# Optimization experiments

Measured on AMD Instinct MI355X. Metric: run time of the kernel, lower is better.

## Reference

```python
import jax, jax.numpy as jnp
import numpy as np

C_FINE, C_MID, C_COARSE = 100, 20, 5
EPS = 1e-12


def setup_inputs() -> dict:
    key = jax.random.key(0)
    k1, k2 = jax.random.split(key)
    N, D = 262144, 128
    representations = jax.random.normal(k1, (N, D), dtype=jnp.float32)
    target_fine = jax.random.randint(k2, (N,), 0, C_FINE, dtype=jnp.int32)
    # nested hierarchy: fine -> mid (5 fines per mid), fine -> coarse (20 fines per coarse)
    fine2mid = (jnp.arange(C_FINE, dtype=jnp.int32) // (C_FINE // C_MID)).astype(jnp.int32)
    fine2coarse = (jnp.arange(C_FINE, dtype=jnp.int32) // (C_FINE // C_COARSE)).astype(jnp.int32)
    return {
        "representations": representations,
        "target_fine": target_fine,
        "fine2mid": fine2mid,
        "fine2coarse": fine2coarse,
    }


def _safe_norm(diff):
    # L2 norm along last axis; eps gives a 0 subgradient at diff==0
    return jnp.sqrt(jnp.sum(diff * diff, axis=-1) + EPS)


def _segment_mean(x, ids, num_segments):
    ones = jnp.ones(x.shape[:1], x.dtype)
    s = jax.ops.segment_sum(x, ids, num_segments=num_segments)
    c = jax.ops.segment_sum(ones, ids, num_segments=num_segments)
    return s / jnp.maximum(c, 1.0)[:, None]


def reference(representations, target_fine, fine2mid, fine2coarse):
    # ---- tree construction (vectorized version of the per-class Python loops) ----
    # fine prototypes: mean of representations per fine class  [C_FINE, D]
    fine_protos = _segment_mean(representations, target_fine, C_FINE)
    # mid prototypes: mean of child fine prototypes  [C_MID, D]
    mid_protos = _segment_mean(fine_protos, fine2mid, C_MID)
    # coarse prototypes: mean of child mid prototypes  [C_COARSE, D]
    mid2coarse = jax.ops.segment_max(fine2coarse, fine2mid, num_segments=C_MID)
    coarse_protos = _segment_mean(mid_protos, mid2coarse, C_COARSE)
    # (the root node contributes ||root - root|| = 0 to every pair, so it is omitted)

    # ---- pairwise tree-path distances over all fine-class pairs ----
    iu, ju = np.triu_indices(C_FINE, k=1)  # static C*(C-1)/2 = 4950 pairs
    ci, cj = fine2coarse[iu], fine2coarse[ju]
    mi, mj = fine2mid[iu], fine2mid[ju]
    tree_d = _safe_norm(coarse_protos[ci] - coarse_protos[cj]) \
           + _safe_norm(mid_protos[mi] - mid_protos[mj])
    # Euclidean distances between fine prototypes
    proto_d = _safe_norm(fine_protos[iu] - fine_protos[ju])

    # ---- CPCC: loss = 1 - Pearson correlation(tree_d, proto_d) ----
    tc = tree_d - jnp.mean(tree_d)
    pc = proto_d - jnp.mean(proto_d)
    corr = jnp.sum(tc * pc) / jnp.sqrt(jnp.sum(tc * tc) * jnp.sum(pc * pc) + EPS)
    return 1.0 - corr
```

## Files before the change

### kernel.cpp

```cpp
#include <hip/hip_runtime.h>
#include <math.h>

#define C_FINE   100
#define C_MID    20
#define C_COARSE 5
#define D        128
#define NROWS    262144
#define NPAIRS   4950
#define NBLK4    78

#define NBS      256
#define NBD      16
#define CAP      4096

#define FP_OFF    0
#define DM_OFF    12800
#define DC_OFF    13200
#define ACC_OFF   13232
#define DONE_OFF  13244
#define FSUM_OFF  13248
#define CUR_OFF   26048
#define RIDX_OFF  26176

__global__ __launch_bounds__(128) void kZ_zero(float* __restrict__ ws) {
    const int t = threadIdx.x;
    if (t < C_FINE) ((int*)ws + CUR_OFF)[t] = 0;
}

__global__ __launch_bounds__(256) void kS_scatter(const int* __restrict__ tgt,
                                                  float* __restrict__ ws) {
    __shared__ int hist[C_FINE];
    __shared__ int cnt[C_FINE];
    __shared__ int gb[C_FINE];
    const int t = threadIdx.x, b = blockIdx.x;
    if (t < C_FINE) { hist[t] = 0; cnt[t] = 0; }
    if (t < 50) ws[FSUM_OFF + b * 50 + t] = 0.f;
    __syncthreads();

    const int4 cs = ((const int4*)tgt)[b * 256 + t];
    atomicAdd(&hist[cs.x], 1); atomicAdd(&hist[cs.y], 1);
    atomicAdd(&hist[cs.z], 1); atomicAdd(&hist[cs.w], 1);
    __syncthreads();

    int* curs = (int*)ws + CUR_OFF;
    if (t < C_FINE && hist[t] > 0) gb[t] = atomicAdd(&curs[t], hist[t]);
    __syncthreads();

    int* ridx = (int*)ws + RIDX_OFF;
    const int r0 = b * 1024 + t * 4;
    int c, s, p;
    c = cs.x; s = atomicAdd(&cnt[c], 1); p = gb[c] + s; if (p < CAP) ridx[c * CAP + p] = r0;
    c = cs.y; s = atomicAdd(&cnt[c], 1); p = gb[c] + s; if (p < CAP) ridx[c * CAP + p] = r0 + 1;
    c = cs.z; s = atomicAdd(&cnt[c], 1); p = gb[c] + s; if (p < CAP) ridx[c * CAP + p] = r0 + 2;
    c = cs.w; s = atomicAdd(&cnt[c], 1); p = gb[c] + s; if (p < CAP) ridx[c * CAP + p] = r0 + 3;
}

__global__ __launch_bounds__(256) void kD_gather(const float* __restrict__ rep,
                                                 float* __restrict__ ws) {
    const int c = blockIdx.x >> 4, j = blockIdx.x & (NBD - 1);
    const int t = threadIdx.x, s = t >> 5, lane = t & 31;
    const int nt = min(((const int*)ws + CUR_OFF)[c], CAP);
    const int b0 = c * CAP;
    const int* ridx = (const int*)ws + RIDX_OFF;
    const float4* rep4 = (const float4*)rep;
    const int STRIDE = NBD * 8;

    float4 a0 = make_float4(0.f, 0.f, 0.f, 0.f);
    float4 a1 = make_float4(0.f, 0.f, 0.f, 0.f);
    int k = j * 8 + s;
    while (k + STRIDE < nt) {
        int r0 = ridx[b0 + k];
        int r1 = ridx[b0 + k + STRIDE];
        float4 v0 = rep4[(size_t)r0 * 32 + lane];
        float4 v1 = rep4[(size_t)r1 * 32 + lane];
        a0.x += v0.x; a0.y += v0.y; a0.z += v0.z; a0.w += v0.w;
        a1.x += v1.x; a1.y += v1.y; a1.z += v1.z; a1.w += v1.w;
        k += 2 * STRIDE;
    }
    if (k < nt) {
        int r0 = ridx[b0 + k];
        float4 v0 = rep4[(size_t)r0 * 32 + lane];
        a0.x += v0.x; a0.y += v0.y; a0.z += v0.z; a0.w += v0.w;
    }
    a0.x += a1.x; a0.y += a1.y; a0.z += a1.z; a0.w += a1.w;

    __shared__ float red[8][128];
    *(float4*)&red[s][lane * 4] = a0;
    __syncthreads();
    if (t < D) {
        float sum = 0.f;
        #pragma unroll
        for (int q = 0; q < 8; ++q) sum += red[q][t];
        atomicAdd(ws + FSUM_OFF + c * D + t, sum);
    }
}

__global__ __launch_bounds__(256) void k3_hier(const int* __restrict__ f2m,
                                               const int* __restrict__ f2c,
                                               float* __restrict__ ws) {
    __shared__ float fineP[C_FINE][D];
    __shared__ float midP[C_MID][D + 1];
    __shared__ float coarP[C_COARSE][D + 1];
    __shared__ int   sf2m[C_FINE], sf2c[C_FINE], m2c[C_MID];
    __shared__ float midCnt[C_MID], coarCnt[C_COARSE];
    __shared__ float sTot[C_FINE];
    const int t = threadIdx.x;

    if (t < C_FINE) {
        sf2m[t] = f2m[t]; sf2c[t] = f2c[t];
        sTot[t] = (float)((const int*)ws + CUR_OFF)[t];
    }
    for (int e = t; e < C_MID * (D + 1); e += 256) ((float*)midP)[e] = 0.f;
    for (int e = t; e < C_COARSE * (D + 1); e += 256) ((float*)coarP)[e] = 0.f;
    __syncthreads();

    for (int e = t; e < C_FINE * D; e += 256) {
        int c = e >> 7, d = e & 127;
        float v = ws[FSUM_OFF + e] / fmaxf(sTot[c], 1.f);
        fineP[c][d] = v;
        ws[FP_OFF + e] = v;
    }
    if (t < C_MID) {
        int cnt = 0, mx = -2147483647;
        for (int f = 0; f < C_FINE; ++f)
            if (sf2m[f] == t) { ++cnt; mx = max(mx, sf2c[f]); }
        midCnt[t] = (float)max(cnt, 1);
        m2c[t] = mx;
    }
    __syncthreads();

    if (t < D) {
        const int d = t;
        for (int f = 0; f < C_FINE; ++f)
            midP[sf2m[f]][d] += fineP[f][d];
        for (int m = 0; m < C_MID; ++m)
            midP[m][d] /= midCnt[m];
    }
    if (t >= 128 && t < 128 + C_COARSE) {
        int cc = t - 128, cnt = 0;
        for (int m = 0; m < C_MID; ++m) if (m2c[m] == cc) ++cnt;
        coarCnt[cc] = (float)max(cnt, 1);
    }
    __syncthreads();

    if (t < D) {
        const int d = t;
        for (int m = 0; m < C_MID; ++m)
            coarP[m2c[m]][d] += midP[m][d];
        for (int cc = 0; cc < C_COARSE; ++cc)
            coarP[cc][d] /= coarCnt[cc];
    }
    __syncthreads();

    for (int e = t; e < C_MID * C_MID; e += 256) {
        int m1 = e / C_MID, m2 = e % C_MID;
        float ss = 0.f;
        #pragma unroll 8
        for (int d = 0; d < D; ++d) {
            float df = midP[m1][d] - midP[m2][d];
            ss += df * df;
        }
        ws[DM_OFF + e] = sqrtf(ss + 1e-12f);
    }
    for (int e = t; e < C_COARSE * C_COARSE; e += 256) {
        int c1 = e / C_COARSE, c2 = e % C_COARSE;
        float ss = 0.f;
        #pragma unroll 8
        for (int d = 0; d < D; ++d) {
            float df = coarP[c1][d] - coarP[c2][d];
            ss += df * df;
        }
        ws[DC_OFF + e] = sqrtf(ss + 1e-12f);
    }
    if (t < 5) ((double*)(ws + ACC_OFF))[t] = 0.0;
    if (t == 5) ((int*)ws + DONE_OFF)[0] = 0;
}

__global__ __launch_bounds__(64) void k45_pairs(float* __restrict__ ws,
                                                const int* __restrict__ f2m,
                                                const int* __restrict__ f2c,
                                                float* __restrict__ out) {
    const int p = blockIdx.x * 64 + threadIdx.x;
    double st = 0, sp = 0, stp = 0, stt = 0, spp = 0;
    if (p < NPAIRS) {
        int i = 0, rem = p;
        while (rem >= C_FINE - 1 - i) { rem -= C_FINE - 1 - i; ++i; }
        int j = i + 1 + rem;

        const float4* Fi = (const float4*)(ws + FP_OFF + i * D);
        const float4* Fj = (const float4*)(ws + FP_OFF + j * D);
        float ss = 0.f;
        #pragma unroll
        for (int k = 0; k < D / 4; ++k) {
            float4 a = Fi[k], b = Fj[k];
            float dx = a.x - b.x, dy = a.y - b.y, dz = a.z - b.z, dw = a.w - b.w;
            ss += dx * dx + dy * dy + dz * dz + dw * dw;
        }
        float proto = sqrtf(ss + 1e-12f);
        float tree  = ws[DC_OFF + f2c[i] * C_COARSE + f2c[j]]
                    + ws[DM_OFF + f2m[i] * C_MID + f2m[j]];
        st = tree; sp = proto;
        stp = (double)tree * (double)proto;
        stt = (double)tree * (double)tree;
        spp = (double)proto * (double)proto;
    }
    for (int off = 32; off > 0; off >>= 1) {
        st  += __shfl_down(st, off);
        sp  += __shfl_down(sp, off);
        stp += __shfl_down(stp, off);
        stt += __shfl_down(stt, off);
        spp += __shfl_down(spp, off);
    }
    if (threadIdx.x == 0) {
        double* acc = (double*)(ws + ACC_OFF);
        atomicAdd(&acc[0], st);
        atomicAdd(&acc[1], sp);
        atomicAdd(&acc[2], stp);
        atomicAdd(&acc[3], stt);
        atomicAdd(&acc[4], spp);
        __threadfence();
        int* done = (int*)ws + DONE_OFF;
        int ticket = atomicAdd(done, 1);
        if (ticket == NBLK4 - 1) {
            double fst  = atomicAdd(&acc[0], 0.0);
            double fsp  = atomicAdd(&acc[1], 0.0);
            double fstp = atomicAdd(&acc[2], 0.0);
            double fstt = atomicAdd(&acc[3], 0.0);
            double fspp = atomicAdd(&acc[4], 0.0);
            const double n = (double)NPAIRS;
            double num = fstp - fst * fsp / n;
            double dtt = fstt - fst * fst / n;
            double dpp = fspp - fsp * fsp / n;
            double corr = num / sqrt(dtt * dpp + 1e-12);
            out[0] = (float)(1.0 - corr);
        }
    }
}

extern "C" void kernel_launch(void* const* d_in, const int* in_sizes, int n_in,
                              void* d_out, int out_size, void* d_ws, size_t ws_size,
                              hipStream_t stream) {
    const float* rep = (const float*)d_in[0];
    const int*   tgt = (const int*)d_in[1];
    const int*   f2m = (const int*)d_in[2];
    const int*   f2c = (const int*)d_in[3];
    float* ws  = (float*)d_ws;
    float* out = (float*)d_out;

    hipLaunchKernelGGL(kZ_zero,    dim3(1),            dim3(128), 0, stream, ws);
    hipLaunchKernelGGL(kS_scatter, dim3(NBS),          dim3(256), 0, stream, tgt, ws);
    hipLaunchKernelGGL(kD_gather,  dim3(C_FINE * NBD), dim3(256), 0, stream, rep, ws);
    hipLaunchKernelGGL(k3_hier,    dim3(1),            dim3(256), 0, stream, f2m, f2c, ws);
    hipLaunchKernelGGL(k45_pairs,  dim3(NBLK4),        dim3(64),  0, stream,
                       ws, f2m, f2c, out);
}
```

Before: 73.97 us.

## Replace counting-sort gather with streaming per-block LDS class accumulation

```diff
diff --git a/kernel.cpp b/kernel.cpp
--- a/kernel.cpp
+++ b/kernel.cpp
@@ -9,90 +9,100 @@
 #define NPAIRS   4950
 #define NBLK4    78
 
-#define NBS      256
-#define NBD      16
-#define CAP      4096
+#define WPG      768
+#define BATCH    16
+#define NBATCH   (NROWS/BATCH)
+#define RG       8
+#define RB       (WPG/RG)
+#define PSTR     12928
 
 #define FP_OFF    0
 #define DM_OFF    12800
 #define DC_OFF    13200
 #define ACC_OFF   13232
 #define DONE_OFF  13244
-#define FSUM_OFF  13248
-#define CUR_OFF   26048
-#define RIDX_OFF  26176
-
-__global__ __launch_bounds__(128) void kZ_zero(float* __restrict__ ws) {
+#define CNT_OFF   13248
+#define FSUM_OFF  13360
+#define PART_OFF  26176
+
+__global__ __launch_bounds__(64) void kAcc(const float* __restrict__ rep,
+                                           const int* __restrict__ tgt,
+                                           float* __restrict__ ws) {
+    __shared__ float acc[C_FINE][D];
+    __shared__ float cnt[C_FINE];
+    const int lane = threadIdx.x;
+    const int wid  = blockIdx.x;
+
+    for (int e = lane; e < C_FINE * D / 4; e += 64)
+        ((float4*)acc)[e] = make_float4(0.f, 0.f, 0.f, 0.f);
+    for (int e = lane; e < C_FINE; e += 64) cnt[e] = 0.f;
+    if (wid == 0) {
+        for (int e = lane; e < 3228; e += 64)
+            ((float4*)(ws + CNT_OFF))[e] = make_float4(0.f, 0.f, 0.f, 0.f);
+    }
+    __syncthreads();
+
+    const float4* rep4 = (const float4*)rep;
+    const int2*   tgt2 = (const int2*)tgt;
+
+    for (int b = wid; b < NBATCH; b += WPG) {
+        const int base = b * BATCH;
+        float4 v[8]; int2 cc[8];
+        #pragma unroll
+        for (int u = 0; u < 8; ++u)
+            v[u] = rep4[(size_t)(base + 2 * u) * 32 + lane];
+        #pragma unroll
+        for (int u = 0; u < 8; ++u)
+            cc[u] = tgt2[base / 2 + u];
+        #pragma unroll
+        for (int u = 0; u < 8; ++u) {
+            const int cA = cc[u].x, cB = cc[u].y;
+            if (cA == cB) {
+                float4 w;
+                w.x = __shfl(v[u].x, lane | 32);
+                w.y = __shfl(v[u].y, lane | 32);
+                w.z = __shfl(v[u].z, lane | 32);
+                w.w = __shfl(v[u].w, lane | 32);
+                if (lane < 32) {
+                    float4 a = *(float4*)&acc[cA][lane * 4];
+                    a.x += v[u].x + w.x; a.y += v[u].y + w.y;
+                    a.z += v[u].z + w.z; a.w += v[u].w + w.w;
+                    *(float4*)&acc[cA][lane * 4] = a;
+                    if (lane == 0) cnt[cA] += 2.f;
+                }
+            } else {
+                const int myc = (lane < 32) ? cA : cB;
+                const int dl  = (lane & 31) * 4;
+                float4 a = *(float4*)&acc[myc][dl];
+                a.x += v[u].x; a.y += v[u].y; a.z += v[u].z; a.w += v[u].w;
+                *(float4*)&acc[myc][dl] = a;
+                if ((lane & 31) == 0) cnt[myc] += 1.f;
+            }
+        }
+    }
+    __syncthreads();
+
+    float* part = ws + PART_OFF + (size_t)wid * PSTR;
+    for (int e = lane; e < C_FINE * D / 4; e += 64)
+        ((float4*)part)[e] = ((const float4*)acc)[e];
+    for (int e = lane; e < C_FINE; e += 64) part[12800 + e] = cnt[e];
+}
+
+__global__ __launch_bounds__(128) void kRed(float* __restrict__ ws) {
+    const int c = blockIdx.x >> 3, g = blockIdx.x & 7;
     const int t = threadIdx.x;
-    if (t < C_FINE) ((int*)ws + CUR_OFF)[t] = 0;
-}
-
-__global__ __launch_bounds__(256) void kS_scatter(const int* __restrict__ tgt,
-                                                  float* __restrict__ ws) {
-    __shared__ int hist[C_FINE];
-    __shared__ int cnt[C_FINE];
-    __shared__ int gb[C_FINE];
-    const int t = threadIdx.x, b = blockIdx.x;
-    if (t < C_FINE) { hist[t] = 0; cnt[t] = 0; }
-    if (t < 50) ws[FSUM_OFF + b * 50 + t] = 0.f;
-    __syncthreads();
-
-    const int4 cs = ((const int4*)tgt)[b * 256 + t];
-    atomicAdd(&hist[cs.x], 1); atomicAdd(&hist[cs.y], 1);
-    atomicAdd(&hist[cs.z], 1); atomicAdd(&hist[cs.w], 1);
-    __syncthreads();
-
-    int* curs = (int*)ws + CUR_OFF;
-    if (t < C_FINE && hist[t] > 0) gb[t] = atomicAdd(&curs[t], hist[t]);
-    __syncthreads();
-
-    int* ridx = (int*)ws + RIDX_OFF;
-    const int r0 = b * 1024 + t * 4;
-    int c, s, p;
-    c = cs.x; s = atomicAdd(&cnt[c], 1); p = gb[c] + s; if (p < CAP) ridx[c * CAP + p] = r0;
-    c = cs.y; s = atomicAdd(&cnt[c], 1); p = gb[c] + s; if (p < CAP) ridx[c * CAP + p] = r0 + 1;
-    c = cs.z; s = atomicAdd(&cnt[c], 1); p = gb[c] + s; if (p < CAP) ridx[c * CAP + p] = r0 + 2;
-    c = cs.w; s = atomicAdd(&cnt[c], 1); p = gb[c] + s; if (p < CAP) ridx[c * CAP + p] = r0 + 3;
-}
-
-__global__ __launch_bounds__(256) void kD_gather(const float* __restrict__ rep,
-                                                 float* __restrict__ ws) {
-    const int c = blockIdx.x >> 4, j = blockIdx.x & (NBD - 1);
-    const int t = threadIdx.x, s = t >> 5, lane = t & 31;
-    const int nt = min(((const int*)ws + CUR_OFF)[c], CAP);
-    const int b0 = c * CAP;
-    const int* ridx = (const int*)ws + RIDX_OFF;
-    const float4* rep4 = (const float4*)rep;
-    const int STRIDE = NBD * 8;
-
-    float4 a0 = make_float4(0.f, 0.f, 0.f, 0.f);
-    float4 a1 = make_float4(0.f, 0.f, 0.f, 0.f);
-    int k = j * 8 + s;
-    while (k + STRIDE < nt) {
-        int r0 = ridx[b0 + k];
-        int r1 = ridx[b0 + k + STRIDE];
-        float4 v0 = rep4[(size_t)r0 * 32 + lane];
-        float4 v1 = rep4[(size_t)r1 * 32 + lane];
-        a0.x += v0.x; a0.y += v0.y; a0.z += v0.z; a0.w += v0.w;
-        a1.x += v1.x; a1.y += v1.y; a1.z += v1.z; a1.w += v1.w;
-        k += 2 * STRIDE;
-    }
-    if (k < nt) {
-        int r0 = ridx[b0 + k];
-        float4 v0 = rep4[(size_t)r0 * 32 + lane];
-        a0.x += v0.x; a0.y += v0.y; a0.z += v0.z; a0.w += v0.w;
-    }
-    a0.x += a1.x; a0.y += a1.y; a0.z += a1.z; a0.w += a1.w;
-
-    __shared__ float red[8][128];
-    *(float4*)&red[s][lane * 4] = a0;
-    __syncthreads();
-    if (t < D) {
-        float sum = 0.f;
-        #pragma unroll
-        for (int q = 0; q < 8; ++q) sum += red[q][t];
-        atomicAdd(ws + FSUM_OFF + c * D + t, sum);
-    }
+    const float* p = ws + PART_OFF + (size_t)(g * RB) * PSTR + c * D + t;
+    float s = 0.f;
+    #pragma unroll 8
+    for (int b = 0; b < RB; ++b) s += p[(size_t)b * PSTR];
+    atomicAdd(ws + FSUM_OFF + c * D + t, s);
+
+    float cl = (t < RB) ? ws[PART_OFF + (size_t)(g * RB + t) * PSTR + 12800 + c] : 0.f;
+    for (int off = 32; off > 0; off >>= 1) cl += __shfl_down(cl, off);
+    __shared__ float r2[2];
+    if ((t & 63) == 0) r2[t >> 6] = cl;
+    __syncthreads();
+    if (t == 0) atomicAdd(ws + CNT_OFF + c, r2[0] + r2[1]);
 }
 
 __global__ __launch_bounds__(256) void k3_hier(const int* __restrict__ f2m,
@@ -108,7 +118,7 @@
 
     if (t < C_FINE) {
         sf2m[t] = f2m[t]; sf2c[t] = f2c[t];
-        sTot[t] = (float)((const int*)ws + CUR_OFF)[t];
+        sTot[t] = ws[CNT_OFF + t];
     }
     for (int e = t; e < C_MID * (D + 1); e += 256) ((float*)midP)[e] = 0.f;
     for (int e = t; e < C_COARSE * (D + 1); e += 256) ((float*)coarP)[e] = 0.f;
@@ -121,10 +131,10 @@
         ws[FP_OFF + e] = v;
     }
     if (t < C_MID) {
-        int cnt = 0, mx = -2147483647;
+        int cntv = 0, mx = -2147483647;
         for (int f = 0; f < C_FINE; ++f)
-            if (sf2m[f] == t) { ++cnt; mx = max(mx, sf2c[f]); }
-        midCnt[t] = (float)max(cnt, 1);
+            if (sf2m[f] == t) { ++cntv; mx = max(mx, sf2c[f]); }
+        midCnt[t] = (float)max(cntv, 1);
         m2c[t] = mx;
     }
     __syncthreads();
@@ -137,9 +147,9 @@
             midP[m][d] /= midCnt[m];
     }
     if (t >= 128 && t < 128 + C_COARSE) {
-        int cc = t - 128, cnt = 0;
-        for (int m = 0; m < C_MID; ++m) if (m2c[m] == cc) ++cnt;
-        coarCnt[cc] = (float)max(cnt, 1);
+        int cc = t - 128, cntv = 0;
+        for (int m = 0; m < C_MID; ++m) if (m2c[m] == cc) ++cntv;
+        coarCnt[cc] = (float)max(cntv, 1);
     }
     __syncthreads();
 
@@ -247,10 +257,9 @@
     float* ws  = (float*)d_ws;
     float* out = (float*)d_out;
 
-    hipLaunchKernelGGL(kZ_zero,    dim3(1),            dim3(128), 0, stream, ws);
-    hipLaunchKernelGGL(kS_scatter, dim3(NBS),          dim3(256), 0, stream, tgt, ws);
-    hipLaunchKernelGGL(kD_gather,  dim3(C_FINE * NBD), dim3(256), 0, stream, rep, ws);
-    hipLaunchKernelGGL(k3_hier,    dim3(1),            dim3(256), 0, stream, f2m, f2c, ws);
-    hipLaunchKernelGGL(k45_pairs,  dim3(NBLK4),        dim3(64),  0, stream,
+    hipLaunchKernelGGL(kAcc,      dim3(WPG),         dim3(64),  0, stream, rep, tgt, ws);
+    hipLaunchKernelGGL(kRed,      dim3(C_FINE * RG), dim3(128), 0, stream, ws);
+    hipLaunchKernelGGL(k3_hier,   dim3(1),           dim3(256), 0, stream, f2m, f2c, ws);
+    hipLaunchKernelGGL(k45_pairs, dim3(NBLK4),       dim3(64),  0, stream,
                        ws, f2m, f2c, out);
 }
```

Measured after the change: 91.51 us. 23.7% more time.
